# Optimization experiments

Hardware: AMD Instinct MI355X
Metric: run time of the kernel (lower is better)

## Reference

```python
import jax, jax.numpy as jnp
import numpy as np
from jax import lax

H = 32  # hidden size


def _lstm_layer(x, Wih, Whh, bih, bhh):
    """x: [B, T, D_in]; returns [B, T, H]. PyTorch gate order i,f,g,o."""
    B = x.shape[0]
    b = bih + bhh  # [4H]
    # precompute input projections for all timesteps: [T, B, 4H]
    xp = jnp.einsum('btd,gd->tbg', x, Wih) + b

    def step(carry, xt):
        h, c = carry
        gates = xt + h @ Whh.T  # [B, 4H]
        i, f, g, o = jnp.split(gates, 4, axis=-1)
        i = jax.nn.sigmoid(i)
        f = jax.nn.sigmoid(f)
        g = jnp.tanh(g)
        o = jax.nn.sigmoid(o)
        c = f * c + i * g
        h = o * jnp.tanh(c)
        return (h, c), h

    init = (jnp.zeros((B, H), x.dtype), jnp.zeros((B, H), x.dtype))
    _, ys = lax.scan(step, init, xp)  # ys: [T, B, H]
    return jnp.swapaxes(ys, 0, 1)


def _lstm5(x, Wih0, Wih_rest, Whh, bih, bhh):
    h = _lstm_layer(x, Wih0, Whh[0], bih[0], bhh[0])
    for l in range(4):  # fixed small layer count
        h = _lstm_layer(h, Wih_rest[l], Whh[l + 1], bih[l + 1], bhh[l + 1])
    return h


def setup_inputs() -> dict:
    key = jax.random.key(0)
    ks = jax.random.split(key, 18)
    s = 1.0 / np.sqrt(H)
    B, T = 16384, 20
    u = lambda k, shp: jax.random.uniform(k, shp, jnp.float32, -s, s)
    return {
        'accel': jax.random.normal(ks[0], (B, T, 3), jnp.float32),
        'gyro': jax.random.normal(ks[1], (B, T, 3), jnp.float32),
        'accel_Wih0': u(ks[2], (4 * H, 3)),
        'accel_Wih_rest': u(ks[3], (4, 4 * H, H)),
        'accel_Whh': u(ks[4], (5, 4 * H, H)),
        'accel_bih': u(ks[5], (5, 4 * H)),
        'accel_bhh': u(ks[6], (5, 4 * H)),
        'gyro_Wih0': u(ks[7], (4 * H, 3)),
        'gyro_Wih_rest': u(ks[8], (4, 4 * H, H)),
        'gyro_Whh': u(ks[9], (5, 4 * H, H)),
        'gyro_bih': u(ks[10], (5, 4 * H)),
        'gyro_bhh': u(ks[11], (5, 4 * H)),
        'fc1_w': u(ks[12], (128, T * H * 2)),
        'fc1_b': u(ks[13], (128,)),
        'fc2_w': u(ks[14], (5, 128)),
        'fc2_b': u(ks[15], (5,)),
    }


def reference(accel, gyro, accel_Wih0, accel_Wih_rest, accel_Whh, accel_bih,
              accel_bhh, gyro_Wih0, gyro_Wih_rest, gyro_Whh, gyro_bih,
              gyro_bhh, fc1_w, fc1_b, fc2_w, fc2_b):
    a = _lstm5(accel, accel_Wih0, accel_Wih_rest, accel_Whh, accel_bih, accel_bhh)
    g = _lstm5(gyro, gyro_Wih0, gyro_Wih_rest, gyro_Whh, gyro_bih, gyro_bhh)
    x = jnp.concatenate([a, g], axis=1)          # [B, 2T, H]
    x = x.reshape(x.shape[0], -1)                # [B, 2*T*H]
    x = jax.nn.relu(x @ fc1_w.T + fc1_b)         # [B, 128]
    return x @ fc2_w.T + fc2_b                   # [B, 5]
```

## Files before the change

kernel.cpp:

```cpp
#include <hip/hip_runtime.h>
#include <math.h>

#define B_TOTAL 16384
#define T_STEPS 20
#define NGRP    1024

typedef __attribute__((ext_vector_type(8))) __bf16 bf16x8;
typedef __attribute__((ext_vector_type(4))) float f32x4;

__device__ __forceinline__ float sigf(float x) {
    return __builtin_amdgcn_rcpf(1.0f + __expf(-x));
}
__device__ __forceinline__ float tanhf_fast(float x) {
    return fmaf(-2.0f, __builtin_amdgcn_rcpf(__expf(2.0f * x) + 1.0f), 1.0f);
}

__device__ __forceinline__ __bf16 bf16_bits(unsigned short s) {
    __bf16 r; __builtin_memcpy(&r, &s, 2); return r;
}
__device__ __forceinline__ void split_trunc(float x, __bf16& hi, __bf16& lo) {
    unsigned u = __float_as_uint(x);
    hi = bf16_bits((unsigned short)(u >> 16));
    float l = x - __uint_as_float(u & 0xFFFF0000u);
    lo = bf16_bits((unsigned short)(__float_as_uint(l) >> 16));
}

__global__ __launch_bounds__(256, 4)
void lstm5_mfma(const float* __restrict__ accel, const float* __restrict__ gyro,
                const float* __restrict__ aWih0, const float* __restrict__ aWihR,
                const float* __restrict__ aWhh,  const float* __restrict__ aBih,
                const float* __restrict__ aBhh,
                const float* __restrict__ gWih0, const float* __restrict__ gWihR,
                const float* __restrict__ gWhh,  const float* __restrict__ gBih,
                const float* __restrict__ gBhh,
                __bf16* __restrict__ Xhi, __bf16* __restrict__ Xlo) {
    const int tid  = threadIdx.x;
    const int w    = tid >> 6;
    const int lane = tid & 63;
    const int e    = lane & 15;
    const int quad = lane >> 4;
    const int sensor = blockIdx.y;
    const int bbase  = blockIdx.x * 16;

    const float* xin  = sensor ? gyro  : accel;
    const float* Wih0 = sensor ? gWih0 : aWih0;
    const float* WihR = sensor ? gWihR : aWihR;
    const float* Whh  = sensor ? gWhh  : aWhh;
    const float* Bih  = sensor ? gBih  : aBih;
    const float* Bhh  = sensor ? gBhh  : aBhh;

    __shared__ __align__(16) __bf16 shi[20 * 512];
    __shared__ __align__(16) __bf16 slo[20 * 512];

    const int ug0 = w * 8 + quad;
    const int ug1 = w * 8 + 4 + quad;

    const int m_row   = lane & 15;
    const int orow_t0 = (m_row & 3) * 32 + (w * 8 + (m_row >> 2));
    const int orow_t1 = (m_row & 3) * 32 + (w * 8 + 4 + (m_row >> 2));

    bf16x8 wih_h0, wih_l0, wih_h1, wih_l1;
    bf16x8 whh_h0, whh_l0, whh_h1, whh_l1;
    f32x4  bias0v, bias1v;
    float  c0 = 0.f, c1 = 0.f;

#define LOAD_FRAG(Wsrc, orow, fh, fl)                         \
    {                                                         \
        const float* p_ = (Wsrc) + (orow) * 32 + quad * 8;    \
        _Pragma("unroll")                                     \
        for (int jj = 0; jj < 8; ++jj) {                      \
            __bf16 h_, l_;                                    \
            split_trunc(p_[jj], h_, l_);                      \
            (fh)[jj] = h_;  (fl)[jj] = l_;                    \
        }                                                     \
    }

#define LOAD_BIAS(l)                                                        \
    {                                                                       \
        _Pragma("unroll")                                                   \
        for (int r = 0; r < 4; ++r) {                                       \
            bias0v[r] = Bih[(l) * 128 + r * 32 + ug0] + Bhh[(l) * 128 + r * 32 + ug0]; \
            bias1v[r] = Bih[(l) * 128 + r * 32 + ug1] + Bhh[(l) * 128 + r * 32 + ug1]; \
        }                                                                   \
    }

#define ACT_STORE(t)                                                        \
    {                                                                       \
        float i0 = sigf(acc0[0]), f0 = sigf(acc0[1]);                       \
        float g0 = tanhf_fast(acc0[2]), o0 = sigf(acc0[3]);                 \
        c0 = f0 * c0 + i0 * g0;                                             \
        float h0 = o0 * tanhf_fast(c0);                                     \
        float i1 = sigf(acc1[0]), f1 = sigf(acc1[1]);                       \
        float g1 = tanhf_fast(acc1[2]), o1 = sigf(acc1[3]);                 \
        c1 = f1 * c1 + i1 * g1;                                             \
        float h1 = o1 * tanhf_fast(c1);                                     \
        __syncthreads();             \
        int i0x = (t) * 512 + w * 128 + e * 8 + quad;                       \
        int i1x = i0x + 4;                                                  \
        __bf16 hh_, ll_;                                                    \
        split_trunc(h0, hh_, ll_);  shi[i0x] = hh_;  slo[i0x] = ll_;        \
        split_trunc(h1, hh_, ll_);  shi[i1x] = hh_;  slo[i1x] = ll_;        \
        __syncthreads();       \
    }

    {
        LOAD_FRAG(Whh, orow_t0, whh_h0, whh_l0);
        LOAD_FRAG(Whh, orow_t1, whh_h1, whh_l1);
        LOAD_BIAS(0);
        float w0reg[2][4][3];
#pragma unroll
        for (int r = 0; r < 4; ++r)
#pragma unroll
            for (int k = 0; k < 3; ++k) {
                w0reg[0][r][k] = Wih0[(r * 32 + ug0) * 3 + k];
                w0reg[1][r][k] = Wih0[(r * 32 + ug1) * 3 + k];
            }
        const float* xrow = xin + (size_t)(bbase + e) * (T_STEPS * 3);

        for (int t = 0; t < T_STEPS; ++t) {
            float x0 = xrow[t * 3 + 0];
            float x1 = xrow[t * 3 + 1];
            float x2 = xrow[t * 3 + 2];
            f32x4 acc0 = bias0v;
            f32x4 acc1 = bias1v;
#pragma unroll
            for (int r = 0; r < 4; ++r) {
                acc0[r] = fmaf(w0reg[0][r][0], x0,
                          fmaf(w0reg[0][r][1], x1,
                          fmaf(w0reg[0][r][2], x2, acc0[r])));
                acc1[r] = fmaf(w0reg[1][r][0], x0,
                          fmaf(w0reg[1][r][1], x1,
                          fmaf(w0reg[1][r][2], x2, acc1[r])));
            }
            if (t > 0) {
                int rb = (t - 1) * 512 + quad * 128 + e * 8;
                bf16x8 bh = *(const bf16x8*)&shi[rb];
                bf16x8 bl = *(const bf16x8*)&slo[rb];
                acc0 = __builtin_amdgcn_mfma_f32_16x16x32_bf16(whh_h0, bh, acc0, 0, 0, 0);
                acc0 = __builtin_amdgcn_mfma_f32_16x16x32_bf16(whh_h0, bl, acc0, 0, 0, 0);
                acc0 = __builtin_amdgcn_mfma_f32_16x16x32_bf16(whh_l0, bh, acc0, 0, 0, 0);
                acc1 = __builtin_amdgcn_mfma_f32_16x16x32_bf16(whh_h1, bh, acc1, 0, 0, 0);
                acc1 = __builtin_amdgcn_mfma_f32_16x16x32_bf16(whh_h1, bl, acc1, 0, 0, 0);
                acc1 = __builtin_amdgcn_mfma_f32_16x16x32_bf16(whh_l1, bh, acc1, 0, 0, 0);
            }
            ACT_STORE(t);
        }
    }

    for (int l = 1; l < 5; ++l) {
        const float* Wi = WihR + (l - 1) * 4096;
        const float* Wh = Whh + l * 4096;
        LOAD_FRAG(Wi, orow_t0, wih_h0, wih_l0);
        LOAD_FRAG(Wi, orow_t1, wih_h1, wih_l1);
        LOAD_FRAG(Wh, orow_t0, whh_h0, whh_l0);
        LOAD_FRAG(Wh, orow_t1, whh_h1, whh_l1);
        LOAD_BIAS(l);
        c0 = 0.f; c1 = 0.f;

        for (int t = 0; t < T_STEPS; ++t) {
            f32x4 acc0, acc1;
            {
                int rb = t * 512 + quad * 128 + e * 8;
                bf16x8 bh = *(const bf16x8*)&shi[rb];
                bf16x8 bl = *(const bf16x8*)&slo[rb];
                acc0 = __builtin_amdgcn_mfma_f32_16x16x32_bf16(wih_h0, bh, bias0v, 0, 0, 0);
                acc0 = __builtin_amdgcn_mfma_f32_16x16x32_bf16(wih_h0, bl, acc0, 0, 0, 0);
                acc0 = __builtin_amdgcn_mfma_f32_16x16x32_bf16(wih_l0, bh, acc0, 0, 0, 0);
                acc1 = __builtin_amdgcn_mfma_f32_16x16x32_bf16(wih_h1, bh, bias1v, 0, 0, 0);
                acc1 = __builtin_amdgcn_mfma_f32_16x16x32_bf16(wih_h1, bl, acc1, 0, 0, 0);
                acc1 = __builtin_amdgcn_mfma_f32_16x16x32_bf16(wih_l1, bh, acc1, 0, 0, 0);
            }
            if (t > 0) {
                int rb = (t - 1) * 512 + quad * 128 + e * 8;
                bf16x8 bh = *(const bf16x8*)&shi[rb];
                bf16x8 bl = *(const bf16x8*)&slo[rb];
                acc0 = __builtin_amdgcn_mfma_f32_16x16x32_bf16(whh_h0, bh, acc0, 0, 0, 0);
                acc0 = __builtin_amdgcn_mfma_f32_16x16x32_bf16(whh_h0, bl, acc0, 0, 0, 0);
                acc0 = __builtin_amdgcn_mfma_f32_16x16x32_bf16(whh_l0, bh, acc0, 0, 0, 0);
                acc1 = __builtin_amdgcn_mfma_f32_16x16x32_bf16(whh_h1, bh, acc1, 0, 0, 0);
                acc1 = __builtin_amdgcn_mfma_f32_16x16x32_bf16(whh_h1, bl, acc1, 0, 0, 0);
                acc1 = __builtin_amdgcn_mfma_f32_16x16x32_bf16(whh_l1, bh, acc1, 0, 0, 0);
            }
            ACT_STORE(t);
        }
    }
    __syncthreads();

    {
        size_t base = ((size_t)(sensor * NGRP + blockIdx.x)) * (20 * 512);
        float4* dh = (float4*)(Xhi + base);
        float4* dl = (float4*)(Xlo + base);
        const float4* sh = (const float4*)shi;
        const float4* sl = (const float4*)slo;
        for (int i = tid; i < 20 * 512 / 8; i += 256) { dh[i] = sh[i]; dl[i] = sl[i]; }
    }
#undef LOAD_FRAG
#undef LOAD_BIAS
#undef ACT_STORE
}

__global__ void w1_prep(const float* __restrict__ w1,
                        __bf16* __restrict__ w1ah, __bf16* __restrict__ w1al) {
    int t = blockIdx.x * blockDim.x + threadIdx.x;
    if (t >= 20480) return;
    int lane = t & 63;
    int ks   = (t >> 6) % 40;
    int mt   = t / (64 * 40);
    int row  = mt * 16 + (lane & 15);
    int col0 = ks * 32 + (lane >> 4) * 8;
    const float* src = w1 + row * 1280 + col0;
#pragma unroll
    for (int j = 0; j < 8; ++j) {
        __bf16 h_, l_;
        split_trunc(src[j], h_, l_);
        w1ah[t * 8 + j] = h_;
        w1al[t * 8 + j] = l_;
    }
}

__global__ __launch_bounds__(256, 4)
void fc_mfma(const __bf16* __restrict__ Xhi, const __bf16* __restrict__ Xlo,
             const __bf16* __restrict__ w1ah, const __bf16* __restrict__ w1al,
             const float* __restrict__ fc1_b, const float* __restrict__ fc2_w,
             const float* __restrict__ fc2_b, float* __restrict__ out) {
    const int tid  = threadIdx.x;
    const int wv   = tid >> 6;
    const int lane = tid & 63;
    const int e    = lane & 15;
    const int quad = lane >> 4;
    const int g    = blockIdx.x;

    __shared__ __align__(16) f32x4 sacc[4][8][64];
    __shared__ float sred[4][16][5];

    f32x4 acc[8];
#pragma unroll
    for (int m = 0; m < 8; ++m) acc[m] = (f32x4){0.f, 0.f, 0.f, 0.f};

    for (int kk = 0; kk < 10; ++kk) {
        int ks = wv * 10 + kk;
        int sensor = ks / 20, t = ks % 20;
        size_t bb = ((size_t)(sensor * NGRP + g)) * (20 * 512) + t * 512 + lane * 8;
        bf16x8 bh = *(const bf16x8*)(Xhi + bb);
        bf16x8 bl = *(const bf16x8*)(Xlo + bb);
#pragma unroll
        for (int m = 0; m < 8; ++m) {
            const __bf16* ap = w1ah + ((size_t)((m * 40 + ks) * 64 + lane)) * 8;
            const __bf16* al = w1al + ((size_t)((m * 40 + ks) * 64 + lane)) * 8;
            bf16x8 ah = *(const bf16x8*)ap;
            bf16x8 av = *(const bf16x8*)al;
            acc[m] = __builtin_amdgcn_mfma_f32_16x16x32_bf16(ah, bh, acc[m], 0, 0, 0);
            acc[m] = __builtin_amdgcn_mfma_f32_16x16x32_bf16(ah, bl, acc[m], 0, 0, 0);
            acc[m] = __builtin_amdgcn_mfma_f32_16x16x32_bf16(av, bh, acc[m], 0, 0, 0);
        }
    }
#pragma unroll
    for (int m = 0; m < 8; ++m) sacc[wv][m][lane] = acc[m];
    __syncthreads();

    float p[5] = {0.f, 0.f, 0.f, 0.f, 0.f};
#pragma unroll
    for (int mm = 0; mm < 2; ++mm) {
        int mt = wv * 2 + mm;
        f32x4 z = sacc[0][mt][lane];
#pragma unroll
        for (int k = 1; k < 4; ++k) {
            f32x4 zz = sacc[k][mt][lane];
#pragma unroll
            for (int r = 0; r < 4; ++r) z[r] += zz[r];
        }
#pragma unroll
        for (int r = 0; r < 4; ++r) {
            int row = mt * 16 + quad * 4 + r;
            float v = fmaxf(z[r] + fc1_b[row], 0.f);
#pragma unroll
            for (int n = 0; n < 5; ++n) p[n] = fmaf(v, fc2_w[n * 128 + row], p[n]);
        }
    }
#pragma unroll
    for (int n = 0; n < 5; ++n) {
        p[n] += __shfl_xor(p[n], 16, 64);
        p[n] += __shfl_xor(p[n], 32, 64);
    }
    if (quad == 0) {
#pragma unroll
        for (int n = 0; n < 5; ++n) sred[wv][e][n] = p[n];
    }
    __syncthreads();
    if (tid < 80) {
        int col = tid / 5, n = tid - col * 5;
        out[(size_t)(g * 16 + col) * 5 + n] =
            sred[0][col][n] + sred[1][col][n] + sred[2][col][n] + sred[3][col][n] + fc2_b[n];
    }
}

extern "C" void kernel_launch(void* const* d_in, const int* in_sizes, int n_in,
                              void* d_out, int out_size, void* d_ws, size_t ws_size,
                              hipStream_t stream) {
    const float* accel  = (const float*)d_in[0];
    const float* gyro   = (const float*)d_in[1];
    const float* aWih0  = (const float*)d_in[2];
    const float* aWihR  = (const float*)d_in[3];
    const float* aWhh   = (const float*)d_in[4];
    const float* aBih   = (const float*)d_in[5];
    const float* aBhh   = (const float*)d_in[6];
    const float* gWih0  = (const float*)d_in[7];
    const float* gWihR  = (const float*)d_in[8];
    const float* gWhh   = (const float*)d_in[9];
    const float* gBih   = (const float*)d_in[10];
    const float* gBhh   = (const float*)d_in[11];
    const float* fc1_w  = (const float*)d_in[12];
    const float* fc1_b  = (const float*)d_in[13];
    const float* fc2_w  = (const float*)d_in[14];
    const float* fc2_b  = (const float*)d_in[15];
    float* out = (float*)d_out;

    const size_t XN = (size_t)2 * NGRP * 20 * 512;
    __bf16* Xhi  = (__bf16*)d_ws;
    __bf16* Xlo  = Xhi + XN;
    __bf16* W1ah = Xlo + XN;
    __bf16* W1al = W1ah + 163840;

    hipLaunchKernelGGL(w1_prep, dim3(80), dim3(256), 0, stream, fc1_w, W1ah, W1al);

    hipLaunchKernelGGL(lstm5_mfma, dim3(NGRP, 2), dim3(256), 0, stream,
                       accel, gyro, aWih0, aWihR, aWhh, aBih, aBhh,
                       gWih0, gWihR, gWhh, gBih, gBhh, Xhi, Xlo);

    hipLaunchKernelGGL(fc_mfma, dim3(NGRP), dim3(256), 0, stream,
                       Xhi, Xlo, W1ah, W1al, fc1_b, fc2_w, fc2_b, out);
}
```

Before: 291.7 us.

## Share reciprocals across gate activations, fold w1 prep into LSTM, retile FC kernel

The LSTM activation step now computes the four gate sigmoids/tanh with a single reciprocal per column via product-of-denominators, and clamps exponent arguments to avoid overflow. Both cell tanh's share one reciprocal too. The fc1 weight split-to-bf16 prep is merged into the first 80 LSTM blocks, removing one kernel launch. The FC kernel is retiled so each block handles two batch groups with a 2x2 wave split (K halves by sensor, M halves), reusing weight fragments across two columns; this adds register pressure and lowers launch occupancy hints.

After: 321.6 us. 1.1x slower.

```diff
diff --git a/kernel.cpp b/kernel.cpp
--- a/kernel.cpp
+++ b/kernel.cpp
@@ -7,13 +7,6 @@
 
 typedef __attribute__((ext_vector_type(8))) __bf16 bf16x8;
 typedef __attribute__((ext_vector_type(4))) float f32x4;
-
-__device__ __forceinline__ float sigf(float x) {
-    return __builtin_amdgcn_rcpf(1.0f + __expf(-x));
-}
-__device__ __forceinline__ float tanhf_fast(float x) {
-    return fmaf(-2.0f, __builtin_amdgcn_rcpf(__expf(2.0f * x) + 1.0f), 1.0f);
-}
 
 __device__ __forceinline__ __bf16 bf16_bits(unsigned short s) {
     __bf16 r; __builtin_memcpy(&r, &s, 2); return r;
@@ -33,6 +26,8 @@
                 const float* __restrict__ gWih0, const float* __restrict__ gWihR,
                 const float* __restrict__ gWhh,  const float* __restrict__ gBih,
                 const float* __restrict__ gBhh,
+                const float* __restrict__ fc1_w,
+                __bf16* __restrict__ w1ah, __bf16* __restrict__ w1al,
                 __bf16* __restrict__ Xhi, __bf16* __restrict__ Xlo) {
     const int tid  = threadIdx.x;
     const int w    = tid >> 6;
@@ -41,6 +36,23 @@
     const int quad = lane >> 4;
     const int sensor = blockIdx.y;
     const int bbase  = blockIdx.x * 16;
+
+    if (sensor == 0 && blockIdx.x < 80) {
+        int idx = blockIdx.x * 256 + tid;
+        int plane = idx & 63;
+        int ks    = (idx >> 6) % 40;
+        int mt    = idx / (64 * 40);
+        int row   = mt * 16 + (plane & 15);
+        int col0  = ks * 32 + (plane >> 4) * 8;
+        const float* src = fc1_w + row * 1280 + col0;
+#pragma unroll
+        for (int j = 0; j < 8; ++j) {
+            __bf16 h_, l_;
+            split_trunc(src[j], h_, l_);
+            w1ah[(size_t)idx * 8 + j] = h_;
+            w1al[(size_t)idx * 8 + j] = l_;
+        }
+    }
 
     const float* xin  = sensor ? gyro  : accel;
     const float* Wih0 = sensor ? gWih0 : aWih0;
@@ -86,14 +98,35 @@
 
 #define ACT_STORE(t)                                                        \
     {                                                                       \
-        float i0 = sigf(acc0[0]), f0 = sigf(acc0[1]);                       \
-        float g0 = tanhf_fast(acc0[2]), o0 = sigf(acc0[3]);                 \
-        c0 = f0 * c0 + i0 * g0;                                             \
-        float h0 = o0 * tanhf_fast(c0);                                     \
-        float i1 = sigf(acc1[0]), f1 = sigf(acc1[1]);                       \
-        float g1 = tanhf_fast(acc1[2]), o1 = sigf(acc1[3]);                 \
-        c1 = f1 * c1 + i1 * g1;                                             \
-        float h1 = o1 * tanhf_fast(c1);                                     \
+        float d1 = 1.f + __expf(fminf(-acc0[0], 17.f));                     \
+        float d2 = 1.f + __expf(fminf(-acc0[1], 17.f));                     \
+        float d3 = 1.f + __expf(fminf(2.f * acc0[2], 17.f));                \
+        float d4 = 1.f + __expf(fminf(-acc0[3], 17.f));                     \
+        float p2 = d1 * d2, p3 = p2 * d3, P = p3 * d4;                      \
+        float s3 = d3 * d4, s2 = d2 * s3;                                   \
+        float R  = __builtin_amdgcn_rcpf(P);                                \
+        float i0 = R * s2;                                                  \
+        float f0 = R * d1 * s3;                                             \
+        float g0 = fmaf(-2.f, R * p2 * d4, 1.f);                            \
+        float o0 = R * p3;                                                  \
+        c0 = fmaf(f0, c0, i0 * g0);                                         \
+        float e1 = 1.f + __expf(fminf(-acc1[0], 17.f));                     \
+        float e2 = 1.f + __expf(fminf(-acc1[1], 17.f));                     \
+        float e3 = 1.f + __expf(fminf(2.f * acc1[2], 17.f));                \
+        float e4 = 1.f + __expf(fminf(-acc1[3], 17.f));                     \
+        float q2 = e1 * e2, q3 = q2 * e3, Q = q3 * e4;                      \
+        float u3 = e3 * e4, u2 = e2 * u3;                                   \
+        float S  = __builtin_amdgcn_rcpf(Q);                                \
+        float i1 = S * u2;                                                  \
+        float f1 = S * e1 * u3;                                             \
+        float g1 = fmaf(-2.f, S * q2 * e4, 1.f);                            \
+        float o1 = S * q3;                                                  \
+        c1 = fmaf(f1, c1, i1 * g1);                                         \
+        float d9 = 1.f + __expf(fminf(2.f * c0, 30.f));                     \
+        float da = 1.f + __expf(fminf(2.f * c1, 30.f));                     \
+        float R2 = __builtin_amdgcn_rcpf(d9 * da);                          \
+        float h0 = fmaf(-2.f, o0 * (R2 * da), o0);                          \
+        float h1 = fmaf(-2.f, o1 * (R2 * d9), o1);                          \
         __syncthreads();             \
         int i0x = (t) * 512 + w * 128 + e * 8 + quad;                       \
         int i1x = i0x + 4;                                                  \
@@ -199,26 +232,7 @@
 #undef ACT_STORE
 }
 
-__global__ void w1_prep(const float* __restrict__ w1,
-                        __bf16* __restrict__ w1ah, __bf16* __restrict__ w1al) {
-    int t = blockIdx.x * blockDim.x + threadIdx.x;
-    if (t >= 20480) return;
-    int lane = t & 63;
-    int ks   = (t >> 6) % 40;
-    int mt   = t / (64 * 40);
-    int row  = mt * 16 + (lane & 15);
-    int col0 = ks * 32 + (lane >> 4) * 8;
-    const float* src = w1 + row * 1280 + col0;
-#pragma unroll
-    for (int j = 0; j < 8; ++j) {
-        __bf16 h_, l_;
-        split_trunc(src[j], h_, l_);
-        w1ah[t * 8 + j] = h_;
-        w1al[t * 8 + j] = l_;
-    }
-}
-
-__global__ __launch_bounds__(256, 4)
+__global__ __launch_bounds__(256, 2)
 void fc_mfma(const __bf16* __restrict__ Xhi, const __bf16* __restrict__ Xlo,
              const __bf16* __restrict__ w1ah, const __bf16* __restrict__ w1al,
              const float* __restrict__ fc1_b, const float* __restrict__ fc2_w,
@@ -228,69 +242,93 @@
     const int lane = tid & 63;
     const int e    = lane & 15;
     const int quad = lane >> 4;
-    const int g    = blockIdx.x;
-
-    __shared__ __align__(16) f32x4 sacc[4][8][64];
-    __shared__ float sred[4][16][5];
-
-    f32x4 acc[8];
-#pragma unroll
-    for (int m = 0; m < 8; ++m) acc[m] = (f32x4){0.f, 0.f, 0.f, 0.f};
-
-    for (int kk = 0; kk < 10; ++kk) {
-        int ks = wv * 10 + kk;
-        int sensor = ks / 20, t = ks % 20;
-        size_t bb = ((size_t)(sensor * NGRP + g)) * (20 * 512) + t * 512 + lane * 8;
-        bf16x8 bh = *(const bf16x8*)(Xhi + bb);
-        bf16x8 bl = *(const bf16x8*)(Xlo + bb);
-#pragma unroll
-        for (int m = 0; m < 8; ++m) {
-            const __bf16* ap = w1ah + ((size_t)((m * 40 + ks) * 64 + lane)) * 8;
-            const __bf16* al = w1al + ((size_t)((m * 40 + ks) * 64 + lane)) * 8;
-            bf16x8 ah = *(const bf16x8*)ap;
-            bf16x8 av = *(const bf16x8*)al;
-            acc[m] = __builtin_amdgcn_mfma_f32_16x16x32_bf16(ah, bh, acc[m], 0, 0, 0);
-            acc[m] = __builtin_amdgcn_mfma_f32_16x16x32_bf16(ah, bl, acc[m], 0, 0, 0);
-            acc[m] = __builtin_amdgcn_mfma_f32_16x16x32_bf16(av, bh, acc[m], 0, 0, 0);
-        }
-    }
-#pragma unroll
-    for (int m = 0; m < 8; ++m) sacc[wv][m][lane] = acc[m];
+    const int kv   = wv & 1;
+    const int mv   = wv >> 1;
+    const int g0   = blockIdx.x * 2;
+
+    __shared__ __align__(16) f32x4 sacc[2][4][2][64];
+    __shared__ float sred[2][2][16][5];
+
+    f32x4 acc[4][2];
+#pragma unroll
+    for (int m = 0; m < 4; ++m)
+#pragma unroll
+        for (int cg = 0; cg < 2; ++cg) acc[m][cg] = (f32x4){0.f, 0.f, 0.f, 0.f};
+
+    for (int kk = 0; kk < 20; ++kk) {
+        int ks = kv * 20 + kk;
+        bf16x8 bh[2], bl[2];
+#pragma unroll
+        for (int cg = 0; cg < 2; ++cg) {
+            size_t bb = ((size_t)(kv * NGRP + g0 + cg)) * (20 * 512) + kk * 512 + lane * 8;
+            bh[cg] = *(const bf16x8*)(Xhi + bb);
+            bl[cg] = *(const bf16x8*)(Xlo + bb);
+        }
+#pragma unroll
+        for (int m = 0; m < 4; ++m) {
+            int mt = mv * 4 + m;
+            size_t ab = ((size_t)((mt * 40 + ks) * 64 + lane)) * 8;
+            bf16x8 ah = *(const bf16x8*)(w1ah + ab);
+            bf16x8 al = *(const bf16x8*)(w1al + ab);
+#pragma unroll
+            for (int cg = 0; cg < 2; ++cg) {
+                acc[m][cg] = __builtin_amdgcn_mfma_f32_16x16x32_bf16(ah, bh[cg], acc[m][cg], 0, 0, 0);
+                acc[m][cg] = __builtin_amdgcn_mfma_f32_16x16x32_bf16(ah, bl[cg], acc[m][cg], 0, 0, 0);
+                acc[m][cg] = __builtin_amdgcn_mfma_f32_16x16x32_bf16(al, bh[cg], acc[m][cg], 0, 0, 0);
+            }
+        }
+    }
+
+    if (kv == 1) {
+#pragma unroll
+        for (int m = 0; m < 4; ++m)
+#pragma unroll
+            for (int cg = 0; cg < 2; ++cg) sacc[mv][m][cg][lane] = acc[m][cg];
+    }
     __syncthreads();
 
-    float p[5] = {0.f, 0.f, 0.f, 0.f, 0.f};
-#pragma unroll
-    for (int mm = 0; mm < 2; ++mm) {
-        int mt = wv * 2 + mm;
-        f32x4 z = sacc[0][mt][lane];
-#pragma unroll
-        for (int k = 1; k < 4; ++k) {
-            f32x4 zz = sacc[k][mt][lane];
-#pragma unroll
-            for (int r = 0; r < 4; ++r) z[r] += zz[r];
-        }
-#pragma unroll
-        for (int r = 0; r < 4; ++r) {
-            int row = mt * 16 + quad * 4 + r;
-            float v = fmaxf(z[r] + fc1_b[row], 0.f);
-#pragma unroll
-            for (int n = 0; n < 5; ++n) p[n] = fmaf(v, fc2_w[n * 128 + row], p[n]);
-        }
-    }
-#pragma unroll
-    for (int n = 0; n < 5; ++n) {
-        p[n] += __shfl_xor(p[n], 16, 64);
-        p[n] += __shfl_xor(p[n], 32, 64);
-    }
-    if (quad == 0) {
-#pragma unroll
-        for (int n = 0; n < 5; ++n) sred[wv][e][n] = p[n];
+    if (kv == 0) {
+        float p[2][5];
+#pragma unroll
+        for (int cg = 0; cg < 2; ++cg)
+#pragma unroll
+            for (int n = 0; n < 5; ++n) p[cg][n] = 0.f;
+#pragma unroll
+        for (int m = 0; m < 4; ++m) {
+            int mt = mv * 4 + m;
+#pragma unroll
+            for (int cg = 0; cg < 2; ++cg) {
+                f32x4 z  = acc[m][cg];
+                f32x4 zz = sacc[mv][m][cg][lane];
+#pragma unroll
+                for (int r = 0; r < 4; ++r) {
+                    int row = mt * 16 + quad * 4 + r;
+                    float v = fmaxf(z[r] + zz[r] + fc1_b[row], 0.f);
+#pragma unroll
+                    for (int n = 0; n < 5; ++n)
+                        p[cg][n] = fmaf(v, fc2_w[n * 128 + row], p[cg][n]);
+                }
+            }
+        }
+#pragma unroll
+        for (int cg = 0; cg < 2; ++cg)
+#pragma unroll
+            for (int n = 0; n < 5; ++n) {
+                p[cg][n] += __shfl_xor(p[cg][n], 16, 64);
+                p[cg][n] += __shfl_xor(p[cg][n], 32, 64);
+            }
+        if (quad == 0) {
+#pragma unroll
+            for (int cg = 0; cg < 2; ++cg)
+#pragma unroll
+                for (int n = 0; n < 5; ++n) sred[mv][cg][e][n] = p[cg][n];
+        }
     }
     __syncthreads();
-    if (tid < 80) {
+    if (tid < 160) {
         int col = tid / 5, n = tid - col * 5;
-        out[(size_t)(g * 16 + col) * 5 + n] =
-            sred[0][col][n] + sred[1][col][n] + sred[2][col][n] + sred[3][col][n] + fc2_b[n];
+        out[((size_t)(blockIdx.x * 32 + col)) * 5 + n] =
+            sred[0][col >> 4][col & 15][n] + sred[1][col >> 4][col & 15][n] + fc2_b[n];
     }
 }
 
@@ -321,12 +359,11 @@
     __bf16* W1ah = Xlo + XN;
     __bf16* W1al = W1ah + 163840;
 
-    hipLaunchKernelGGL(w1_prep, dim3(80), dim3(256), 0, stream, fc1_w, W1ah, W1al);
-
     hipLaunchKernelGGL(lstm5_mfma, dim3(NGRP, 2), dim3(256), 0, stream,
                        accel, gyro, aWih0, aWihR, aWhh, aBih, aBhh,
-                       gWih0, gWihR, gWhh, gBih, gBhh, Xhi, Xlo);
-
-    hipLaunchKernelGGL(fc_mfma, dim3(NGRP), dim3(256), 0, stream,
+                       gWih0, gWihR, gWhh, gBih, gBhh,
+                       fc1_w, W1ah, W1al, Xhi, Xlo);
+
+    hipLaunchKernelGGL(fc_mfma, dim3(B_TOTAL / 32), dim3(256), 0, stream,
                        Xhi, Xlo, W1ah, W1al, fc1_b, fc2_w, fc2_b, out);
 }
```
